# Kernel tuning notes

Hardware: AMD Instinct MI355X
Metric: run time of the kernel (lower is better)

The kernel has to match this reference:

```python
import jax, jax.numpy as jnp
import numpy as np

KERNEL_SIZE = 5
BANDWIDTH = 1.0
N_KERNELS = KERNEL_SIZE * KERNEL_SIZE - 1  # 24, center tap excluded
PAD = KERNEL_SIZE // 2


def _offsets():
    # one-hot kernel index for slot i skips the center position
    offs = []
    for i in range(N_KERNELS):
        idx = i if i < N_KERNELS // 2 else i + 1
        offs.append((idx // KERNEL_SIZE, idx % KERNEL_SIZE))
    return offs


def setup_inputs() -> dict:
    key = jax.random.key(0)
    X = jax.random.normal(key, (4, 3, 512, 512), dtype=jnp.float32)
    return {"X": X}


def reference(X) -> jnp.ndarray:
    B, C, H, W = X.shape
    # zero padding matches Conv2d(padding=k//2, bias=False) with one-hot weights
    Xp = jnp.pad(X, ((0, 0), (0, 0), (PAD, PAD), (PAD, PAD)))
    # the grouped one-hot conv is just a neighbor-shift gather:
    # Xj[:, :, i, h, w] = Xp[:, :, h + r_i, w + c_i]
    Xj = jnp.stack([Xp[:, :, r:r + H, c:c + W] for (r, c) in _offsets()], axis=2)
    Xi = X[:, :, None, :, :]  # [B, C, 1, H, W]
    inv = 1.0 / (2.0 * BANDWIDTH * BANDWIDTH)
    K = jnp.exp(-((Xj - Xi) ** 2) * inv)  # [B, C, n_kernels, H, W]
    return K
```

## Files before the change

### kernel.cpp

```cpp
#include <hip/hip_runtime.h>


#define HH 512
#define WW 512
#define NPLANES 12
#define NK 24

typedef float f32x4 __attribute__((ext_vector_type(4)));

extern "C" __device__ float __builtin_amdgcn_exp2f(float);

__global__ __launch_bounds__(256) void gauss_mask_kernel(
    const float* __restrict__ X, float* __restrict__ out)
{
    const int tid = blockIdx.x * blockDim.x + threadIdx.x;
    const int p   = tid >> 16;
    const int rem = tid & 65535;
    const int h   = rem >> 7;
    const int w0  = (rem & 127) << 2;

    const float* Xp = X + (size_t)p * (HH * WW);

    const f32x4 xi4 = *reinterpret_cast<const f32x4*>(Xp + (size_t)h * WW + w0);
    float xiv[4] = {xi4.x, xi4.y, xi4.z, xi4.w};

    float rows[5][8];
    #pragma unroll
    for (int dr = 0; dr < 5; ++dr) {
        const int hh = h + dr - 2;
        const bool rok = (hh >= 0) && (hh < HH);
        const float* rptr = Xp + (size_t)hh * WW;
        #pragma unroll
        for (int j = 0; j < 8; ++j) {
            const int ww = w0 + j - 2;
            rows[dr][j] = (rok && ww >= 0 && ww < WW) ? rptr[ww] : 0.0f;
        }
    }

    const float c = -0.5f * 1.44269504088896340736f;

    float* outp = out + (size_t)p * NK * HH * WW + (size_t)h * WW + w0;

    #pragma unroll
    for (int k = 0; k < NK; ++k) {
        const int idx = (k < 12) ? k : k + 1;
        const int dr = idx / 5;
        const int dc = idx % 5;
        f32x4 v;
        #pragma unroll
        for (int i = 0; i < 4; ++i) {
            const float d = rows[dr][dc + i] - xiv[i];
            v[i] = __builtin_amdgcn_exp2f(d * d * c);
        }
        __builtin_nontemporal_store(v, reinterpret_cast<f32x4*>(outp + (size_t)k * (HH * WW)));
    }
}

extern "C" void kernel_launch(void* const* d_in, const int* in_sizes, int n_in,
                              void* d_out, int out_size, void* d_ws, size_t ws_size,
                              hipStream_t stream) {
    const float* X = (const float*)d_in[0];
    float* out = (float*)d_out;

    const int total = NPLANES * HH * (WW / 4);
    const int block = 256;
    const int grid = total / block;
    gauss_mask_kernel<<<grid, block, 0, stream>>>(X, out);
}
```

Before: 55.68 us.

## Split work across output kernel slices with one tap per block

Each block now handles a single neighbor offset (grid y = tap index), and a template specialization per tap loads the center and neighbor values with vector loads and shuffles instead of 40 scalar loads per thread. Each thread writes one 16-byte output vector, so there are many more threads in flight to cover store latency. The cost is that input rows are re-read 24 times, relying on L2 cache, and block size grows to 512.

```diff
diff --git a/kernel.cpp b/kernel.cpp
--- a/kernel.cpp
+++ b/kernel.cpp
@@ -3,56 +3,102 @@
 
 #define HH 512
 #define WW 512
-#define NPLANES 12
 #define NK 24
+#define HW (HH * WW)
 
 typedef float f32x4 __attribute__((ext_vector_type(4)));
 
 extern "C" __device__ float __builtin_amdgcn_exp2f(float);
 
-__global__ __launch_bounds__(256) void gauss_mask_kernel(
+template <int DR, int DC>
+__device__ __forceinline__ void do_case(const float* __restrict__ Xp,
+                                        float* __restrict__ kp,
+                                        int rem )
+{
+    const float c = -0.5f * 1.44269504088896340736f;
+    const int wcol = rem & 127;
+    const int ci   = rem << 2;
+
+    const f32x4 xc = *reinterpret_cast<const f32x4*>(Xp + ci);
+
+    f32x4 nb;
+    const int h  = rem >> 7;
+    const int hh = h + DR - 2;
+    if ((DR == 2) || (hh >= 0 && hh < HH)) {
+        const int ni = ci + (DR - 2) * WW;
+        if constexpr (DC == 2) {
+            nb = *reinterpret_cast<const f32x4*>(Xp + ni);
+        } else if constexpr (DC < 2) {
+            const bool wl = (wcol > 0);
+            const f32x4 qC = *reinterpret_cast<const f32x4*>(Xp + ni);
+            const f32x4 qA = *reinterpret_cast<const f32x4*>(Xp + ni + (wl ? -4 : 0));
+            const float A2 = wl ? qA[2] : 0.0f;
+            const float A3 = wl ? qA[3] : 0.0f;
+            if constexpr (DC == 0) {
+                nb[0] = A2; nb[1] = A3; nb[2] = qC[0]; nb[3] = qC[1];
+            } else {
+                nb[0] = A3; nb[1] = qC[0]; nb[2] = qC[1]; nb[3] = qC[2];
+            }
+        } else {
+            const bool wr = (wcol < 127);
+            const f32x4 qC = *reinterpret_cast<const f32x4*>(Xp + ni);
+            const f32x4 qB = *reinterpret_cast<const f32x4*>(Xp + ni + (wr ? 4 : 0));
+            const float B0 = wr ? qB[0] : 0.0f;
+            const float B1 = wr ? qB[1] : 0.0f;
+            if constexpr (DC == 3) {
+                nb[0] = qC[1]; nb[1] = qC[2]; nb[2] = qC[3]; nb[3] = B0;
+            } else {
+                nb[0] = qC[2]; nb[1] = qC[3]; nb[2] = B0; nb[3] = B1;
+            }
+        }
+    } else {
+        nb[0] = nb[1] = nb[2] = nb[3] = 0.0f;
+    }
+
+    f32x4 v;
+    #pragma unroll
+    for (int i = 0; i < 4; ++i) {
+        const float d = nb[i] - xc[i];
+        v[i] = __builtin_amdgcn_exp2f(d * d * c);
+    }
+    __builtin_nontemporal_store(v, reinterpret_cast<f32x4*>(kp + ci));
+}
+
+__global__ __launch_bounds__(512) void gauss_mask_kernel(
     const float* __restrict__ X, float* __restrict__ out)
 {
-    const int tid = blockIdx.x * blockDim.x + threadIdx.x;
-    const int p   = tid >> 16;
-    const int rem = tid & 65535;
-    const int h   = rem >> 7;
-    const int w0  = (rem & 127) << 2;
+    const int p   = blockIdx.x >> 7;
+    const int rem = ((blockIdx.x & 127) << 9) | threadIdx.x;
+    const int k   = blockIdx.y;
 
-    const float* Xp = X + (size_t)p * (HH * WW);
+    const float* Xp = X + (size_t)p * HW;
+    float* kp = out + ((size_t)p * NK + k) * HW;
 
-    const f32x4 xi4 = *reinterpret_cast<const f32x4*>(Xp + (size_t)h * WW + w0);
-    float xiv[4] = {xi4.x, xi4.y, xi4.z, xi4.w};
-
-    float rows[5][8];
-    #pragma unroll
-    for (int dr = 0; dr < 5; ++dr) {
-        const int hh = h + dr - 2;
-        const bool rok = (hh >= 0) && (hh < HH);
-        const float* rptr = Xp + (size_t)hh * WW;
-        #pragma unroll
-        for (int j = 0; j < 8; ++j) {
-            const int ww = w0 + j - 2;
-            rows[dr][j] = (rok && ww >= 0 && ww < WW) ? rptr[ww] : 0.0f;
-        }
-    }
-
-    const float c = -0.5f * 1.44269504088896340736f;
-
-    float* outp = out + (size_t)p * NK * HH * WW + (size_t)h * WW + w0;
-
-    #pragma unroll
-    for (int k = 0; k < NK; ++k) {
-        const int idx = (k < 12) ? k : k + 1;
-        const int dr = idx / 5;
-        const int dc = idx % 5;
-        f32x4 v;
-        #pragma unroll
-        for (int i = 0; i < 4; ++i) {
-            const float d = rows[dr][dc + i] - xiv[i];
-            v[i] = __builtin_amdgcn_exp2f(d * d * c);
-        }
-        __builtin_nontemporal_store(v, reinterpret_cast<f32x4*>(outp + (size_t)k * (HH * WW)));
+    switch (k) {
+        case  0: do_case<0, 0>(Xp, kp, rem); break;
+        case  1: do_case<0, 1>(Xp, kp, rem); break;
+        case  2: do_case<0, 2>(Xp, kp, rem); break;
+        case  3: do_case<0, 3>(Xp, kp, rem); break;
+        case  4: do_case<0, 4>(Xp, kp, rem); break;
+        case  5: do_case<1, 0>(Xp, kp, rem); break;
+        case  6: do_case<1, 1>(Xp, kp, rem); break;
+        case  7: do_case<1, 2>(Xp, kp, rem); break;
+        case  8: do_case<1, 3>(Xp, kp, rem); break;
+        case  9: do_case<1, 4>(Xp, kp, rem); break;
+        case 10: do_case<2, 0>(Xp, kp, rem); break;
+        case 11: do_case<2, 1>(Xp, kp, rem); break;
+        case 12: do_case<2, 3>(Xp, kp, rem); break;
+        case 13: do_case<2, 4>(Xp, kp, rem); break;
+        case 14: do_case<3, 0>(Xp, kp, rem); break;
+        case 15: do_case<3, 1>(Xp, kp, rem); break;
+        case 16: do_case<3, 2>(Xp, kp, rem); break;
+        case 17: do_case<3, 3>(Xp, kp, rem); break;
+        case 18: do_case<3, 4>(Xp, kp, rem); break;
+        case 19: do_case<4, 0>(Xp, kp, rem); break;
+        case 20: do_case<4, 1>(Xp, kp, rem); break;
+        case 21: do_case<4, 2>(Xp, kp, rem); break;
+        case 22: do_case<4, 3>(Xp, kp, rem); break;
+        case 23: do_case<4, 4>(Xp, kp, rem); break;
     }
 }
 
@@ -62,8 +108,6 @@
     const float* X = (const float*)d_in[0];
     float* out = (float*)d_out;
 
-    const int total = NPLANES * HH * (WW / 4);
-    const int block = 256;
-    const int grid = total / block;
-    gauss_mask_kernel<<<grid, block, 0, stream>>>(X, out);
+    dim3 grid(1536, NK);
+    gauss_mask_kernel<<<grid, 512, 0, stream>>>(X, out);
 }
```

Result: faster. 53.19 us (-4.5%).
